# Performance work log

Measured on AMD Instinct MI355X. Metric: run time of the kernel, lower is better.

The kernel has to match this reference:

```python
import jax, jax.numpy as jnp
import numpy as np

NUM_NODE_TYPES = 8
HIDDEN = 64
D = 4
N_NODES = 100000
N_EDGES = 3200000
LN_EPS = 1e-5


def setup_inputs() -> dict:
    key = jax.random.key(0)
    ks = jax.random.split(key, 8)
    total_in = 2 * NUM_NODE_TYPES
    out_dim = D * D
    x = jax.random.normal(ks[0], (N_NODES, 16), dtype=jnp.float32)
    edge_index = jax.random.randint(ks[1], (2, N_EDGES), 0, N_NODES, dtype=jnp.int64)
    node_types = jax.random.randint(ks[2], (N_NODES,), 0, NUM_NODE_TYPES, dtype=jnp.int64)
    # LayerNorm params
    ln_g = jnp.ones((total_in,), dtype=jnp.float32)
    ln_b = jnp.zeros((total_in,), dtype=jnp.float32)
    # Linear layers (kaiming-ish init)
    W1 = jax.random.normal(ks[3], (total_in, HIDDEN), dtype=jnp.float32) * (1.0 / np.sqrt(total_in))
    b1 = jnp.zeros((HIDDEN,), dtype=jnp.float32)
    W2 = jax.random.normal(ks[4], (HIDDEN, out_dim), dtype=jnp.float32) * (1.0 / np.sqrt(HIDDEN))
    b2 = jnp.zeros((out_dim,), dtype=jnp.float32)
    return {"x": x, "edge_index": edge_index, "node_types": node_types,
            "ln_g": ln_g, "ln_b": ln_b, "W1": W1, "b1": b1, "W2": W2, "b2": b2}


def reference(x, edge_index, node_types, ln_g, ln_b, W1, b1, W2, b2):
    row, col = edge_index[0], edge_index[1]
    # one-hot node types then per-edge gather of src/tgt types
    onehot = jax.nn.one_hot(node_types, NUM_NODE_TYPES, dtype=jnp.float32)  # [N, T]
    h = jnp.concatenate([onehot[row], onehot[col]], axis=-1)  # [E, 2T]
    # LayerNorm
    mu = jnp.mean(h, axis=-1, keepdims=True)
    var = jnp.mean(jnp.square(h - mu), axis=-1, keepdims=True)
    hn = (h - mu) * jax.lax.rsqrt(var + LN_EPS) * ln_g + ln_b
    # MLP
    h1 = jax.nn.relu(hn @ W1 + b1)          # [E, HIDDEN]
    h_sheaf = (h1 @ W2 + b2).reshape(-1, D, D)  # [E, d, d]
    attention_maps = jax.nn.softmax(h_sheaf, axis=-1)
    sheaf_maps = jnp.eye(D, dtype=h_sheaf.dtype)[None] - attention_maps
    return sheaf_maps
```

## Files before the change

kernel.cpp:

```cpp
#include <hip/hip_runtime.h>
#include <math.h>

#define NUM_T   8
#define TIN     16
#define HID     64
#define OUTD    16
#define LN_EPS  1e-5f

#define N_PACK_U32 12500

typedef float f32x4 __attribute__((ext_vector_type(4)));

__global__ __launch_bounds__(256) void
prep_kernel(const int* __restrict__ ntypes, int n_nodes,
            const float* __restrict__ ln_g,
            const float* __restrict__ ln_b,
            const float* __restrict__ W1,
            const float* __restrict__ b1,
            const float* __restrict__ W2,
            const float* __restrict__ b2,
            f32x4* __restrict__ table4,
            unsigned int* __restrict__ packed)
{
    const int t = threadIdx.x;
    const int g = blockIdx.x * 256 + t;

    if (g < N_PACK_U32) {
        unsigned int w = 0;
        int n0 = g * 8;
        #pragma unroll
        for (int j = 0; j < 8; ++j) {
            int n = n0 + j;
            unsigned int ty = (n < n_nodes) ? (unsigned int)ntypes[n] : 0u;
            w |= (ty & 7u) << (j * 4);
        }
        packed[g] = w;
    }

    if (blockIdx.x != 0) return;

    __shared__ float sW1[TIN * HID];
    __shared__ float sW2[HID * OUTD];
    __shared__ float sb1[HID];
    __shared__ float sg[TIN], sb[TIN], sb2[OUTD];

    for (int i = t; i < TIN * HID; i += 256) sW1[i] = W1[i];
    for (int i = t; i < HID * OUTD; i += 256) sW2[i] = W2[i];
    if (t < HID) sb1[t] = b1[t];
    if (t < TIN) { sg[t] = ln_g[t]; sb[t] = ln_b[t]; }
    if (t < OUTD) sb2[t] = b2[t];
    __syncthreads();

    const int p  = t >> 2;
    const int kg = t & 3;
    const int ts = p >> 3;
    const int tt = p & 7;

    const float mu = 2.0f / 16.0f;
    float var = 0.0f;
    #pragma unroll
    for (int j = 0; j < TIN; ++j) {
        float h = (j == ts || j == (8 + tt)) ? 1.0f : 0.0f;
        float d = h - mu;
        var += d * d;
    }
    var *= (1.0f / 16.0f);
    const float inv = rsqrtf(var + LN_EPS);

    float hn[TIN];
    #pragma unroll
    for (int j = 0; j < TIN; ++j) {
        float h = (j == ts || j == (8 + tt)) ? 1.0f : 0.0f;
        hn[j] = (h - mu) * inv * sg[j] + sb[j];
    }

    float s[OUTD];
    #pragma unroll
    for (int o = 0; o < OUTD; ++o) s[o] = 0.0f;

    const int k0 = kg * 16;
    for (int k = k0; k < k0 + 16; ++k) {
        float a = sb1[k];
        #pragma unroll
        for (int j = 0; j < TIN; ++j) a += hn[j] * sW1[j * HID + k];
        a = fmaxf(a, 0.0f);
        #pragma unroll
        for (int o = 0; o < OUTD; ++o) s[o] += a * sW2[k * OUTD + o];
    }

    #pragma unroll
    for (int o = 0; o < OUTD; ++o) {
        s[o] += __shfl_xor(s[o], 1);
        s[o] += __shfl_xor(s[o], 2);
        s[o] += sb2[o];
    }

    const int r = kg;
    float s0 = s[4*r+0], s1 = s[4*r+1], s2 = s[4*r+2], s3 = s[4*r+3];
    float m  = fmaxf(fmaxf(s0, s1), fmaxf(s2, s3));
    float e0 = expf(s0 - m), e1 = expf(s1 - m),
          e2 = expf(s2 - m), e3 = expf(s3 - m);
    float rs = 1.0f / (e0 + e1 + e2 + e3);
    f32x4 outv;
    outv.x = (r == 0 ? 1.0f : 0.0f) - e0 * rs;
    outv.y = (r == 1 ? 1.0f : 0.0f) - e1 * rs;
    outv.z = (r == 2 ? 1.0f : 0.0f) - e2 * rs;
    outv.w = (r == 3 ? 1.0f : 0.0f) - e3 * rs;
    table4[p * 4 + r] = outv;
}

__global__ __launch_bounds__(256) void
scatter_edges_kernel(const int* __restrict__ row,
                     const int* __restrict__ col,
                     const unsigned int* __restrict__ packed,
                     const f32x4* __restrict__ table4,
                     f32x4* __restrict__ out4,
                     int E)
{
    __shared__ f32x4 lds_table[64 * 5];
    __shared__ unsigned int nt_lds[N_PACK_U32];

    const int t = threadIdx.x;

    {
        int p = t >> 2, q = t & 3;
        lds_table[p * 5 + q] = table4[t];
    }
    {
        const uint4* src4 = (const uint4*)packed;
        uint4* dst4 = (uint4*)nt_lds;
        for (int i = t; i < N_PACK_U32 / 4; i += 256) dst4[i] = src4[i];
        for (int i = (N_PACK_U32 & ~3) + t; i < N_PACK_U32; i += 256)
            nt_lds[i] = packed[i];
    }
    __syncthreads();

    const int q      = t & 3;
    const int lane_e = t >> 2;
    const int stride = gridDim.x * 64;

    for (int e = blockIdx.x * 64 + lane_e; e < E; e += stride) {
        int r = row[e];
        int c = col[e];
        unsigned int wr = nt_lds[r >> 3];
        unsigned int wc = nt_lds[c >> 3];
        int tr = (wr >> ((r & 7) * 4)) & 7;
        int tc = (wc >> ((c & 7) * 4)) & 7;
        int pair = (tr << 3) | tc;
        f32x4 v = lds_table[pair * 5 + q];
        __builtin_nontemporal_store(v, &out4[e * 4 + q]);
    }
}

extern "C" void kernel_launch(void* const* d_in, const int* in_sizes, int n_in,
                              void* d_out, int out_size, void* d_ws, size_t ws_size,
                              hipStream_t stream)
{
    const int*   edge_index = (const int*)d_in[1];
    const int*   ntypes     = (const int*)d_in[2];
    const float* ln_g       = (const float*)d_in[3];
    const float* ln_b       = (const float*)d_in[4];
    const float* W1         = (const float*)d_in[5];
    const float* b1         = (const float*)d_in[6];
    const float* W2         = (const float*)d_in[7];
    const float* b2         = (const float*)d_in[8];

    const int E = in_sizes[1] / 2;
    const int N = in_sizes[2];

    f32x4*        table4 = (f32x4*)d_ws;
    unsigned int* packed = (unsigned int*)((char*)d_ws + 4096);

    const int prep_blocks = (N_PACK_U32 + 255) / 256;
    prep_kernel<<<prep_blocks, 256, 0, stream>>>(
        ntypes, N, ln_g, ln_b, W1, b1, W2, b2, table4, packed);

    const int blocks = 512;
    scatter_edges_kernel<<<blocks, 256, 0, stream>>>(
        edge_index, edge_index + E, packed,
        table4, (f32x4*)d_out, E);
}
```

Baseline: 53.71 us.

## Split edge scatter into pair-index pass and chunked byte-index store pass

Replaces the single scatter kernel with two kernels. The first reads row/col as int4 vectors, looks up packed node types in LDS and writes one byte per edge holding the type-pair index. The second loads a 4096-edge chunk of those bytes into LDS and writes the 64-byte output per edge with fully coalesced nontemporal stores, no longer bound by index-gather latency. This adds an extra launch plus an extra write and read of E bytes, and it needs workspace large enough for the pair buffer; otherwise the old single-kernel path is used.

New measurement: 65.03 us. 21.1% more time.

```diff
diff --git a/kernel.cpp b/kernel.cpp
--- a/kernel.cpp
+++ b/kernel.cpp
@@ -8,6 +8,7 @@
 #define LN_EPS  1e-5f
 
 #define N_PACK_U32 12500
+#define CHUNK      4096
 
 typedef float f32x4 __attribute__((ext_vector_type(4)));
 
@@ -110,6 +111,85 @@
 }
 
 __global__ __launch_bounds__(256) void
+pair_kernel(const int* __restrict__ row,
+            const int* __restrict__ col,
+            const unsigned int* __restrict__ packed,
+            unsigned int* __restrict__ pairs_u32,
+            int n_units)
+{
+    __shared__ unsigned int nt_lds[N_PACK_U32];
+    const int t = threadIdx.x;
+    {
+        const uint4* s4 = (const uint4*)packed;
+        uint4* d4 = (uint4*)nt_lds;
+        for (int i = t; i < N_PACK_U32 / 4; i += 256) d4[i] = s4[i];
+        for (int i = (N_PACK_U32 & ~3) + t; i < N_PACK_U32; i += 256)
+            nt_lds[i] = packed[i];
+    }
+    __syncthreads();
+
+    const int stride = gridDim.x * 256;
+    const int4* row4 = (const int4*)row;
+    const int4* col4 = (const int4*)col;
+
+    for (int u = blockIdx.x * 256 + t; u < n_units; u += stride) {
+        int4 rv = row4[u];
+        int4 cv = col4[u];
+        int rr[4] = {rv.x, rv.y, rv.z, rv.w};
+        int cc[4] = {cv.x, cv.y, cv.z, cv.w};
+        unsigned int outw = 0;
+        #pragma unroll
+        for (int j = 0; j < 4; ++j) {
+            int r = rr[j], c = cc[j];
+            unsigned int tr = (nt_lds[r >> 3] >> ((r & 7) * 4)) & 7u;
+            unsigned int tc = (nt_lds[c >> 3] >> ((c & 7) * 4)) & 7u;
+            outw |= ((tr << 3) | tc) << (j * 8);
+        }
+        pairs_u32[u] = outw;
+    }
+}
+
+__global__ __launch_bounds__(256) void
+store_kernel(const unsigned int* __restrict__ pairs_u32,
+             const f32x4* __restrict__ table4,
+             f32x4* __restrict__ out4,
+             int E)
+{
+    __shared__ f32x4 lds_table[64 * 5];
+    __shared__ unsigned char pair_lds[CHUNK];
+
+    const int t = threadIdx.x;
+    {
+        int p = t >> 2, q = t & 3;
+        lds_table[p * 5 + q] = table4[t];
+    }
+    const int base = blockIdx.x * CHUNK;
+    {
+        unsigned int* pl32 = (unsigned int*)pair_lds;
+        const int n_units = (E + 3) >> 2;
+        #pragma unroll
+        for (int i = t; i < CHUNK / 4; i += 256) {
+            int idx = (base >> 2) + i;
+            pl32[i] = (idx < n_units) ? pairs_u32[idx] : 0u;
+        }
+    }
+    __syncthreads();
+
+    #pragma unroll 8
+    for (int i = 0; i < (CHUNK * 4) / 256; ++i) {
+        int slot = i * 256 + t;
+        int el   = slot >> 2;
+        int q    = slot & 3;
+        int e    = base + el;
+        if (e < E) {
+            int p = pair_lds[el];
+            f32x4 v = lds_table[p * 5 + q];
+            __builtin_nontemporal_store(v, &out4[e * 4 + q]);
+        }
+    }
+}
+
+__global__ __launch_bounds__(256) void
 scatter_edges_kernel(const int* __restrict__ row,
                      const int* __restrict__ col,
                      const unsigned int* __restrict__ packed,
@@ -119,9 +199,7 @@
 {
     __shared__ f32x4 lds_table[64 * 5];
     __shared__ unsigned int nt_lds[N_PACK_U32];
-
-    const int t = threadIdx.x;
-
+    const int t = threadIdx.x;
     {
         int p = t >> 2, q = t & 3;
         lds_table[p * 5 + q] = table4[t];
@@ -170,13 +248,22 @@
 
     f32x4*        table4 = (f32x4*)d_ws;
     unsigned int* packed = (unsigned int*)((char*)d_ws + 4096);
+    unsigned int* pairs  = (unsigned int*)((char*)d_ws + 65536);
 
     const int prep_blocks = (N_PACK_U32 + 255) / 256;
     prep_kernel<<<prep_blocks, 256, 0, stream>>>(
         ntypes, N, ln_g, ln_b, W1, b1, W2, b2, table4, packed);
 
-    const int blocks = 512;
-    scatter_edges_kernel<<<blocks, 256, 0, stream>>>(
-        edge_index, edge_index + E, packed,
-        table4, (f32x4*)d_out, E);
-}
+    if (ws_size >= (size_t)65536 + (size_t)E + 16) {
+        const int n_units = (E + 3) >> 2;
+        pair_kernel<<<512, 256, 0, stream>>>(
+            edge_index, edge_index + E, packed, pairs, n_units);
+
+        const int blocks = (E + CHUNK - 1) / CHUNK;
+        store_kernel<<<blocks, 256, 0, stream>>>(
+            pairs, table4, (f32x4*)d_out, E);
+    } else {
+        scatter_edges_kernel<<<512, 256, 0, stream>>>(
+            edge_index, edge_index + E, packed, table4, (f32x4*)d_out, E);
+    }
+}
```

## Use 1024-thread blocks with per-lane edge loads and shuffle-distributed stores

Applied to the files above, without the earlier changes.

Grows the scatter kernel's blocks from 256 to 1024 threads. Each lane now loads one edge's row and col indices, so index reads are fully coalesced, and the resolved type pairs reach the four-lane store groups through wave shuffles. Regular stores replace the nontemporal stores, and the packed node-type table is still copied into LDS once per block. The ~50KB of LDS per block plus 1024 threads may limit occupancy to one block per CU, and the scalar tail copy of the packed array was dropped.

Result: faster. 51.16 us (-4.8%).

```diff
diff --git a/kernel.cpp b/kernel.cpp
--- a/kernel.cpp
+++ b/kernel.cpp
@@ -109,7 +109,7 @@
     table4[p * 4 + r] = outv;
 }
 
-__global__ __launch_bounds__(256) void
+__global__ __launch_bounds__(1024) void
 scatter_edges_kernel(const int* __restrict__ row,
                      const int* __restrict__ col,
                      const unsigned int* __restrict__ packed,
@@ -122,33 +122,41 @@
 
     const int t = threadIdx.x;
 
-    {
+    if (t < 256) {
         int p = t >> 2, q = t & 3;
         lds_table[p * 5 + q] = table4[t];
     }
     {
-        const uint4* src4 = (const uint4*)packed;
-        uint4* dst4 = (uint4*)nt_lds;
-        for (int i = t; i < N_PACK_U32 / 4; i += 256) dst4[i] = src4[i];
-        for (int i = (N_PACK_U32 & ~3) + t; i < N_PACK_U32; i += 256)
-            nt_lds[i] = packed[i];
+        const uint4* s4 = (const uint4*)packed;
+        uint4* d4 = (uint4*)nt_lds;
+        for (int i = t; i < N_PACK_U32 / 4; i += 1024) d4[i] = s4[i];
     }
     __syncthreads();
 
-    const int q      = t & 3;
-    const int lane_e = t >> 2;
-    const int stride = gridDim.x * 64;
+    const int lane = t & 63;
+    const int wid  = t >> 6;
+    const int q    = lane & 3;
+    const int sub  = lane >> 2;
+    const int stride = gridDim.x * 1024;
 
-    for (int e = blockIdx.x * 64 + lane_e; e < E; e += stride) {
-        int r = row[e];
-        int c = col[e];
-        unsigned int wr = nt_lds[r >> 3];
-        unsigned int wc = nt_lds[c >> 3];
-        int tr = (wr >> ((r & 7) * 4)) & 7;
-        int tc = (wc >> ((c & 7) * 4)) & 7;
-        int pair = (tr << 3) | tc;
-        f32x4 v = lds_table[pair * 5 + q];
-        __builtin_nontemporal_store(v, &out4[e * 4 + q]);
+    for (int base = blockIdx.x * 1024 + wid * 64; base < E; base += stride) {
+        int e  = base + lane;
+        int ec = (e < E) ? e : (E - 1);
+        int r = row[ec];
+        int c = col[ec];
+        unsigned int tr = (nt_lds[r >> 3] >> ((r & 7) * 4)) & 7u;
+        unsigned int tc = (nt_lds[c >> 3] >> ((c & 7) * 4)) & 7u;
+        int pair = (int)((tr << 3) | tc);
+
+        #pragma unroll
+        for (int j = 0; j < 4; ++j) {
+            int src = j * 16 + sub;
+            int pj  = __shfl(pair, src, 64);
+            int ej  = base + src;
+            if (ej < E) {
+                out4[ej * 4 + q] = lds_table[pj * 5 + q];
+            }
+        }
     }
 }
 
@@ -176,7 +184,7 @@
         ntypes, N, ln_g, ln_b, W1, b1, W2, b2, table4, packed);
 
     const int blocks = 512;
-    scatter_edges_kernel<<<blocks, 256, 0, stream>>>(
+    scatter_edges_kernel<<<blocks, 1024, 0, stream>>>(
         edge_index, edge_index + E, packed,
         table4, (f32x4*)d_out, E);
 }
```
